# Kernel optimization log

Measured on AMD Instinct MI355X. Metric: run time of the kernel, lower is better.

The kernel has to match this reference:

```python
import jax, jax.numpy as jnp
import numpy as np

D = 128
N_DRUG = 100000
N_PROT = 50000
E_DD, E_DP, E_PD = 800000, 600000, 600000
EPS = 1e-5


def setup_inputs() -> dict:
    key = jax.random.key(0)
    ks = jax.random.split(key, 19)
    f32 = jnp.float32
    return {
        "x_drug": jax.random.normal(ks[0], (N_DRUG, D), f32),
        "x_prot": jax.random.normal(ks[1], (N_PROT, D), f32),
        "Wagg_dd": jax.random.normal(ks[2], (D, D), f32) * 0.05,
        "Wagg_dp": jax.random.normal(ks[3], (D, D), f32) * 0.05,
        "Wagg_pd": jax.random.normal(ks[4], (D, D), f32) * 0.05,
        "W_drug": jax.random.normal(ks[5], (D, 2 * D), f32) * 0.05,
        "b_drug": jax.random.normal(ks[6], (D,), f32) * 0.01,
        "W_prot": jax.random.normal(ks[7], (D, 2 * D), f32) * 0.05,
        "b_prot": jax.random.normal(ks[8], (D,), f32) * 0.01,
        "g_drug": jnp.ones((D,), f32),
        "be_drug": jnp.zeros((D,), f32),
        "g_prot": jnp.ones((D,), f32),
        "be_prot": jnp.zeros((D,), f32),
        "ei_dd_src": jax.random.randint(ks[9], (E_DD,), 0, N_DRUG, jnp.int64 if jax.config.jax_enable_x64 else jnp.int32),
        "ei_dd_dst": jax.random.randint(ks[10], (E_DD,), 0, N_DRUG),
        "ei_dp_src": jax.random.randint(ks[11], (E_DP,), 0, N_DRUG),
        "ei_dp_dst": jax.random.randint(ks[12], (E_DP,), 0, N_PROT),
        "ei_pd_src": jax.random.randint(ks[13], (E_PD,), 0, N_PROT),
        "ei_pd_dst": jax.random.randint(ks[14], (E_PD,), 0, N_DRUG),
    }


def _rel_agg(x_src, W_agg, src_idx, dst_idx, n_dst):
    # gather -> per-relation Linear (no bias) + ReLU -> scatter-mean
    h = jax.nn.relu(x_src[src_idx] @ W_agg.T)            # [E, D]
    s = jax.ops.segment_sum(h, dst_idx, num_segments=n_dst)
    c = jax.ops.segment_sum(jnp.ones((src_idx.shape[0],), h.dtype), dst_idx, num_segments=n_dst)
    return s / jnp.maximum(c, 1.0)[:, None]


def _layernorm(x, g, b):
    mu = jnp.mean(x, axis=-1, keepdims=True)
    var = jnp.mean(jnp.square(x - mu), axis=-1, keepdims=True)
    return (x - mu) * jax.lax.rsqrt(var + EPS) * g + b


def _node_update(h_self, h_agg, W, b, g, be):
    h = jax.nn.relu(jnp.concatenate([h_self, h_agg], axis=-1) @ W.T + b)
    return _layernorm(h + h_self, g, be)  # dropout is identity in eval


def reference(x_drug, x_prot, Wagg_dd, Wagg_dp, Wagg_pd, W_drug, b_drug,
              W_prot, b_prot, g_drug, be_drug, g_prot, be_prot,
              ei_dd_src, ei_dd_dst, ei_dp_src, ei_dp_dst, ei_pd_src, ei_pd_dst):
    agg_dd = _rel_agg(x_drug, Wagg_dd, ei_dd_src, ei_dd_dst, N_DRUG)
    agg_pd = _rel_agg(x_prot, Wagg_pd, ei_pd_src, ei_pd_dst, N_DRUG)
    agg_drug = (agg_dd + agg_pd) * 0.5                   # mean over relations into 'drug'
    agg_prot = _rel_agg(x_drug, Wagg_dp, ei_dp_src, ei_dp_dst, N_PROT)
    out_drug = _node_update(x_drug, agg_drug, W_drug, b_drug, g_drug, be_drug)
    out_prot = _node_update(x_prot, agg_prot, W_prot, b_prot, g_prot, be_prot)
    # pack the per-type outputs into one array [N_DRUG + N_PROT, D]
    return jnp.concatenate([out_drug, out_prot], axis=0)
```

## Files before the change

kernel.cpp:

```cpp
#include <hip/hip_runtime.h>

#define D 128
#define ND 100000
#define NP 50000
#define NE_DD 800000
#define NE_DP 600000
#define NE_PD 600000
#define NE_TOT 2000000

#define NTOT 250000
#define NBC 490
#define NC 250880
#define CHUNKA 4096
#define NBLKA 489
#define CHUNKIT 16
#define SEGCAP 8192

#define TF_BD 782
#define TF_BP 196
#define NU_BD 391
#define NU_BP 196

typedef __bf16 bf16;
typedef __attribute__((ext_vector_type(8))) __bf16 bf16x8;
typedef __attribute__((ext_vector_type(2))) __bf16 bf16x2;
typedef __attribute__((ext_vector_type(4))) float f32x4;
typedef __attribute__((ext_vector_type(2))) float f32x2;

#define OFF_WDD   0UL
#define OFF_WDP   32768UL
#define OFF_WPD   65536UL
#define OFF_WDRUG 98304UL
#define OFF_WPROT 163840UL
#define OFF_YDD   229376UL
#define OFF_YDP   (OFF_YDD + 25600000UL)
#define OFF_YPD   (OFF_YDP + 25600000UL)
#define OFF_AGGD  (OFF_YPD + 12800000UL)
#define OFF_AGGP  (OFF_AGGD + 25600000UL)
#define OFF_BCNT  (OFF_AGGP + 12800000UL)
#define OFF_GCUR  (OFF_BCNT + 2048UL)
#define OFF_CBASE (OFF_GCUR + 2048UL)
#define OFF_RP    (OFF_CBASE + 2048UL)
#define OFF_PAIRS (OFF_RP + 1003520UL)
#define OFF_POOL  (OFF_PAIRS + 16000000UL)

__global__ __launch_bounds__(256) void prep_kernel(
    const float* __restrict__ w0, const float* __restrict__ w1,
    const float* __restrict__ w2, const float* __restrict__ w3,
    const float* __restrict__ w4,
    bf16* __restrict__ o0, bf16* __restrict__ o1, bf16* __restrict__ o2,
    bf16* __restrict__ o3, bf16* __restrict__ o4,
    const int* __restrict__ dd_dst, const int* __restrict__ pd_dst,
    const int* __restrict__ dp_dst, int* __restrict__ bcnt)
{
    int m = blockIdx.y;
    int t = threadIdx.x;
    if (m == 5) {
        __shared__ int h[NBC];
        for (int i = t; i < NBC; i += 256) h[i] = 0;
        __syncthreads();
        for (int e = blockIdx.x * 256 + t; e < NE_TOT; e += 128 * 256) {
            int didx;
            if (e < NE_DD) didx = dd_dst[e];
            else if (e < NE_DD + NE_PD) didx = ND + pd_dst[e - NE_DD];
            else didx = 2 * ND + dp_dst[e - NE_DD - NE_PD];
            atomicAdd(&h[didx >> 9], 1);
        }
        __syncthreads();
        for (int i = t; i < NBC; i += 256)
            if (h[i]) atomicAdd(&bcnt[i], h[i]);
        return;
    }
    int i = blockIdx.x * 256 + t;
    const float* src; bf16* dst; int n; bool perm;
    switch (m) {
        case 0: src = w0; dst = o0; n = D * D; perm = false; break;
        case 1: src = w1; dst = o1; n = D * D; perm = false; break;
        case 2: src = w2; dst = o2; n = D * D; perm = false; break;
        case 3: src = w3; dst = o3; n = D * 2 * D; perm = true; break;
        default: src = w4; dst = o4; n = D * 2 * D; perm = true; break;
    }
    if (i < n) {
        int si = i;
        if (perm) {
            int col = i & 255;
            if (col >= 128) {
                int p = col - 128;
                si = (i & ~255) | (128 + (p & 7) * 16 + (p >> 3));
            }
        }
        dst[i] = (bf16)src[si];
    }
}

__global__ __launch_bounds__(256) void scan_kernel(
    const int* __restrict__ bcnt, int* __restrict__ cbase, int* __restrict__ gcur)
{
    __shared__ int ps[256];
    int t = threadIdx.x;
    int i0 = 2 * t, i1 = 2 * t + 1;
    int c0 = (i0 < NBC) ? bcnt[i0] : 0;
    int c1 = (i1 < NBC) ? bcnt[i1] : 0;
    ps[t] = c0 + c1;
    __syncthreads();
#pragma unroll
    for (int off = 1; off < 256; off <<= 1) {
        int add = (t >= off) ? ps[t - off] : 0;
        __syncthreads();
        ps[t] += add;
        __syncthreads();
    }
    int excl = ps[t] - (c0 + c1);
    if (i0 <= NBC) cbase[i0] = excl;
    if (i0 < NBC) gcur[i0] = excl;
    if (i1 < NBC) { cbase[i1] = excl + c0; gcur[i1] = excl + c0; }
}

__device__ __forceinline__ bf16x8 load_a_f32(const float* __restrict__ xr)
{
    float4 f0 = *(const float4*)xr;
    float4 f1 = *(const float4*)(xr + 4);
    bf16x8 a;
    a[0] = (bf16)f0.x; a[1] = (bf16)f0.y; a[2] = (bf16)f0.z; a[3] = (bf16)f0.w;
    a[4] = (bf16)f1.x; a[5] = (bf16)f1.y; a[6] = (bf16)f1.z; a[7] = (bf16)f1.w;
    return a;
}

__device__ __forceinline__ void transform_drug(
    const float* __restrict__ x, const bf16* __restrict__ W1,
    const bf16* __restrict__ W2, bf16* __restrict__ y1, bf16* __restrict__ y2,
    int blk)
{
    int lane = threadIdx.x & 63;
    int wave = threadIdx.x >> 6;
    int q = lane >> 4, c = lane & 15;
    int mb = blk * 128 + wave * 32;

    f32x4 acc1[2][8], acc2[2][8];
#pragma unroll
    for (int mt = 0; mt < 2; mt++)
#pragma unroll
        for (int nt = 0; nt < 8; nt++) { acc1[mt][nt] = 0; acc2[mt][nt] = 0; }

#pragma unroll
    for (int kb = 0; kb < 4; kb++) {
        int k = kb * 32 + q * 8;
        bf16x8 a[2];
#pragma unroll
        for (int mt = 0; mt < 2; mt++) {
            int row = min(mb + mt * 16 + c, ND - 1);
            a[mt] = load_a_f32(x + (long)row * D + k);
        }
#pragma unroll
        for (int nt = 0; nt < 8; nt++) {
            bf16x8 b1 = *(const bf16x8*)(W1 + (nt * 16 + c) * D + k);
            bf16x8 b2 = *(const bf16x8*)(W2 + (nt * 16 + c) * D + k);
#pragma unroll
            for (int mt = 0; mt < 2; mt++) {
                acc1[mt][nt] = __builtin_amdgcn_mfma_f32_16x16x32_bf16(a[mt], b1, acc1[mt][nt], 0, 0, 0);
                acc2[mt][nt] = __builtin_amdgcn_mfma_f32_16x16x32_bf16(a[mt], b2, acc2[mt][nt], 0, 0, 0);
            }
        }
    }
#pragma unroll
    for (int mt = 0; mt < 2; mt++)
#pragma unroll
        for (int r = 0; r < 4; r++) {
            int row = mb + mt * 16 + q * 4 + r;
            if (row < ND) {
                bf16x8 o1, o2;
#pragma unroll
                for (int nt = 0; nt < 8; nt++) {
                    o1[nt] = (bf16)fmaxf(acc1[mt][nt][r], 0.f);
                    o2[nt] = (bf16)fmaxf(acc2[mt][nt][r], 0.f);
                }
                *(bf16x8*)(y1 + (long)row * D + c * 8) = o1;
                *(bf16x8*)(y2 + (long)row * D + c * 8) = o2;
            }
        }
}

__device__ __forceinline__ void transform_prot(
    const float* __restrict__ x, const bf16* __restrict__ W1,
    bf16* __restrict__ y1, int blk)
{
    int lane = threadIdx.x & 63;
    int wave = threadIdx.x >> 6;
    int q = lane >> 4, c = lane & 15;
    int mb = blk * 256 + wave * 64;

    f32x4 acc[4][8];
#pragma unroll
    for (int mt = 0; mt < 4; mt++)
#pragma unroll
        for (int nt = 0; nt < 8; nt++) acc[mt][nt] = 0;

#pragma unroll
    for (int kb = 0; kb < 4; kb++) {
        int k = kb * 32 + q * 8;
        bf16x8 a[4];
#pragma unroll
        for (int mt = 0; mt < 4; mt++) {
            int row = min(mb + mt * 16 + c, NP - 1);
            a[mt] = load_a_f32(x + (long)row * D + k);
        }
#pragma unroll
        for (int nt = 0; nt < 8; nt++) {
            bf16x8 b1 = *(const bf16x8*)(W1 + (nt * 16 + c) * D + k);
#pragma unroll
            for (int mt = 0; mt < 4; mt++)
                acc[mt][nt] = __builtin_amdgcn_mfma_f32_16x16x32_bf16(a[mt], b1, acc[mt][nt], 0, 0, 0);
        }
    }
#pragma unroll
    for (int mt = 0; mt < 4; mt++)
#pragma unroll
        for (int r = 0; r < 4; r++) {
            int row = mb + mt * 16 + q * 4 + r;
            if (row < NP) {
                bf16x8 o1;
#pragma unroll
                for (int nt = 0; nt < 8; nt++)
                    o1[nt] = (bf16)fmaxf(acc[mt][nt][r], 0.f);
                *(bf16x8*)(y1 + (long)row * D + c * 8) = o1;
            }
        }
}

__device__ __forceinline__ void binA_body(
    int blk,
    const int* __restrict__ dd_src, const int* __restrict__ dd_dst,
    const int* __restrict__ pd_src, const int* __restrict__ pd_dst,
    const int* __restrict__ dp_src, const int* __restrict__ dp_dst,
    int* __restrict__ gcur, unsigned* __restrict__ pairs)
{
    __shared__ int h[NBC];
    __shared__ int gb[NBC];
    __shared__ int2 pr[CHUNKA];
    __shared__ unsigned short rk[CHUNKA];
    for (int i = threadIdx.x; i < NBC; i += 256) h[i] = 0;
    __syncthreads();
    int base = blk * CHUNKA;
    for (int it = 0; it < CHUNKIT; it++) {
        int idx = it * 256 + threadIdx.x;
        int e = base + idx;
        int didx = -1, sv = 0;
        if (e < NE_TOT) {
            if (e < NE_DD) { didx = dd_dst[e]; sv = dd_src[e]; }
            else if (e < NE_DD + NE_PD) { int u = e - NE_DD; didx = ND + pd_dst[u]; sv = pd_src[u]; }
            else { int u = e - NE_DD - NE_PD; didx = 2 * ND + dp_dst[u]; sv = dp_src[u]; }
            rk[idx] = (unsigned short)atomicAdd(&h[didx >> 9], 1);
        }
        pr[idx] = make_int2(didx, sv);
    }
    __syncthreads();
    for (int b = threadIdx.x; b < NBC; b += 256) {
        int c = h[b];
        gb[b] = c ? atomicAdd(&gcur[b], c) : 0;
    }
    __syncthreads();
    for (int it = 0; it < CHUNKIT; it++) {
        int idx = it * 256 + threadIdx.x;
        int2 p = pr[idx];
        if (p.x >= 0)
            pairs[gb[p.x >> 9] + rk[idx]] =
                ((unsigned)(p.x & 511) << 17) | (unsigned)p.y;
    }
}

__global__ __launch_bounds__(256, 2) void stage2_kernel(
    const float* __restrict__ x_drug, const float* __restrict__ x_prot,
    const bf16* __restrict__ Wdd, const bf16* __restrict__ Wdp,
    const bf16* __restrict__ Wpd,
    bf16* __restrict__ y_dd, bf16* __restrict__ y_dp, bf16* __restrict__ y_pd,
    const int* __restrict__ dd_src, const int* __restrict__ dd_dst,
    const int* __restrict__ pd_src, const int* __restrict__ pd_dst,
    const int* __restrict__ dp_src, const int* __restrict__ dp_dst,
    int* __restrict__ gcur, unsigned* __restrict__ pairs)
{
    int blk = blockIdx.x;
    if (blk < NBLKA) {
        binA_body(blk, dd_src, dd_dst, pd_src, pd_dst, dp_src, dp_dst,
                  gcur, pairs);
        return;
    }
    blk -= NBLKA;
    if (blk < TF_BD)
        transform_drug(x_drug, Wdd, Wdp, y_dd, y_dp, blk);
    else
        transform_prot(x_prot, Wpd, y_pd, blk - TF_BD);
}

__global__ __launch_bounds__(256) void sortB_kernel(
    const int* __restrict__ cbase, const unsigned* __restrict__ pairs,
    int* __restrict__ pool, int* __restrict__ rp)
{
    __shared__ int h[512];
    __shared__ int excl[512];
    __shared__ int ps[256];
    __shared__ unsigned short rk[SEGCAP];
    __shared__ int outl[SEGCAP];

    int b = blockIdx.x;
    int s0 = cbase[b], s1 = cbase[b + 1];
    int n = s1 - s0;
    if (n > SEGCAP) n = SEGCAP;
    int t = threadIdx.x;
    h[t] = 0; h[t + 256] = 0;
    __syncthreads();

    for (int i = t; i < n; i += 256) {
        unsigned p = pairs[s0 + i];
        rk[i] = (unsigned short)atomicAdd(&h[p >> 17], 1);
    }
    __syncthreads();

    int c0 = h[2 * t], c1 = h[2 * t + 1];
    ps[t] = c0 + c1;
    __syncthreads();
#pragma unroll
    for (int off = 1; off < 256; off <<= 1) {
        int add = (t >= off) ? ps[t - off] : 0;
        __syncthreads();
        ps[t] += add;
        __syncthreads();
    }
    int pe = ps[t] - (c0 + c1);
    excl[2 * t] = pe;
    excl[2 * t + 1] = pe + c0;
    __syncthreads();

    int nb = b * 512;
    rp[nb + 2 * t] = s0 + excl[2 * t];
    rp[nb + 2 * t + 1] = s0 + excl[2 * t + 1];

    for (int i = t; i < n; i += 256) {
        unsigned p = pairs[s0 + i];
        outl[excl[p >> 17] + rk[i]] = (int)(p & 0x1FFFFu);
    }
    __syncthreads();
    for (int i = t; i < n; i += 256)
        pool[s0 + i] = outl[i];
}

__device__ __forceinline__ void acc2(unsigned u, f32x2* acc)
{
    union { unsigned u; float f; } lo, hi;
    lo.u = u << 16;
    hi.u = u & 0xFFFF0000u;
    f32x2 d; d.x = lo.f; d.y = hi.f;
    *acc += d;
}

__device__ __forceinline__ void acc_seg(
    const int* __restrict__ pool, int s, int e,
    const unsigned* __restrict__ y, int lane, f32x2* acc)
{
    int j = s;
    for (; j + 8 <= e; j += 8) {
        unsigned u[8];
#pragma unroll
        for (int t = 0; t < 8; t++)
            u[t] = y[(long)pool[j + t] * 64 + lane];
#pragma unroll
        for (int t = 0; t < 8; t++) acc2(u[t], acc);
    }
    if (j + 4 <= e) {
        unsigned u[4];
#pragma unroll
        for (int t = 0; t < 4; t++)
            u[t] = y[(long)pool[j + t] * 64 + lane];
#pragma unroll
        for (int t = 0; t < 4; t++) acc2(u[t], acc);
        j += 4;
    }
    if (j + 2 <= e) {
        unsigned u0 = y[(long)pool[j] * 64 + lane];
        unsigned u1 = y[(long)pool[j + 1] * 64 + lane];
        acc2(u0, acc); acc2(u1, acc);
        j += 2;
    }
    if (j < e)
        acc2(y[(long)pool[j] * 64 + lane], acc);
}

__global__ __launch_bounds__(256) void gather_kernel(
    const int* __restrict__ rp, const int* __restrict__ pool,
    const unsigned* __restrict__ y_dd, const unsigned* __restrict__ y_pd,
    const unsigned* __restrict__ y_dp,
    bf16* __restrict__ agg_d, bf16* __restrict__ agg_p)
{
    int wid = blockIdx.x * 4 + (threadIdx.x >> 6);
    int lane = threadIdx.x & 63;

    if (wid < ND) {
        int g = wid;
        int s1 = rp[g], e1 = rp[g + 1];
        int s2 = rp[ND + g], e2 = rp[ND + g + 1];
        f32x2 a; a.x = 0.f; a.y = 0.f;
        f32x2 b; b.x = 0.f; b.y = 0.f;
        acc_seg(pool, s1, e1, y_dd, lane, &a);
        acc_seg(pool, s2, e2, y_pd, lane, &b);
        float i1 = 0.5f / (float)max(e1 - s1, 1);
        float i2 = 0.5f / (float)max(e2 - s2, 1);
        f32x2 r = a * i1 + b * i2;
        bf16x2 o; o[0] = (bf16)r.x; o[1] = (bf16)r.y;
        *(bf16x2*)(agg_d + (long)g * D + lane * 2) = o;
    } else if (wid < ND + NP) {
        int p = wid - ND;
        int s1 = rp[2 * ND + p], e1 = rp[2 * ND + p + 1];
        f32x2 a; a.x = 0.f; a.y = 0.f;
        acc_seg(pool, s1, e1, y_dp, lane, &a);
        float i1 = 1.0f / (float)max(e1 - s1, 1);
        f32x2 r = a * i1;
        bf16x2 o; o[0] = (bf16)r.x; o[1] = (bf16)r.y;
        *(bf16x2*)(agg_p + (long)p * D + lane * 2) = o;
    }
}

__device__ __forceinline__ void node_update_body(
    const float* __restrict__ x, const bf16* __restrict__ agg,
    const bf16* __restrict__ W, const float* __restrict__ b,
    const float* __restrict__ g, const float* __restrict__ be,
    float* __restrict__ out, int M, int blk)
{
    int lane = threadIdx.x & 63;
    int wave = threadIdx.x >> 6;
    int q = lane >> 4, c = lane & 15;
    int mb = blk * 256 + wave * 64;

    f32x4 acc[4][8];
#pragma unroll
    for (int mt = 0; mt < 4; mt++)
#pragma unroll
        for (int nt = 0; nt < 8; nt++) acc[mt][nt] = 0;

#pragma unroll
    for (int kb = 0; kb < 8; kb++) {
        bf16x8 a[4];
#pragma unroll
        for (int mt = 0; mt < 4; mt++) {
            int row = min(mb + mt * 16 + c, M - 1);
            if (kb < 4)
                a[mt] = load_a_f32(x + (long)row * D + kb * 32 + q * 8);
            else
                a[mt] = *(const bf16x8*)(agg + (long)row * D + (kb - 4) * 32 + q * 8);
        }
#pragma unroll
        for (int nt = 0; nt < 8; nt++) {
            bf16x8 bw = *(const bf16x8*)(W + (nt * 16 + c) * (2 * D) + kb * 32 + q * 8);
#pragma unroll
            for (int mt = 0; mt < 4; mt++)
                acc[mt][nt] = __builtin_amdgcn_mfma_f32_16x16x32_bf16(a[mt], bw, acc[mt][nt], 0, 0, 0);
        }
    }

    float bv[8], gv[8], bev[8];
#pragma unroll
    for (int nt = 0; nt < 8; nt++) {
        int col = nt * 16 + c;
        bv[nt] = b[col]; gv[nt] = g[col]; bev[nt] = be[col];
    }
#pragma unroll
    for (int mt = 0; mt < 4; mt++)
#pragma unroll
        for (int r = 0; r < 4; r++) {
            int row = mb + mt * 16 + q * 4 + r;
            int rowc = min(row, M - 1);
            const float* xr = x + (long)rowc * D + c;
            float v[8];
            float sum = 0.f, sq = 0.f;
#pragma unroll
            for (int nt = 0; nt < 8; nt++) {
                float h = fmaxf(acc[mt][nt][r] + bv[nt], 0.f);
                float t = h + xr[nt * 16];
                v[nt] = t; sum += t; sq += t * t;
            }
#pragma unroll
            for (int m = 1; m < 16; m <<= 1) {
                sum += __shfl_xor(sum, m, 64);
                sq  += __shfl_xor(sq,  m, 64);
            }
            float mu   = sum * (1.f / 128.f);
            float var  = sq  * (1.f / 128.f) - mu * mu;
            float rstd = rsqrtf(var + 1e-5f);
            if (row < M) {
                float* op = out + (long)row * D + c;
#pragma unroll
                for (int nt = 0; nt < 8; nt++)
                    op[nt * 16] = (v[nt] - mu) * rstd * gv[nt] + bev[nt];
            }
        }
}

__global__ __launch_bounds__(256, 2) void node_update_kernel(
    const float* __restrict__ x_drug, const float* __restrict__ x_prot,
    const bf16* __restrict__ agg_d, const bf16* __restrict__ agg_p,
    const bf16* __restrict__ Wdrug, const float* __restrict__ b_drug,
    const float* __restrict__ g_drug, const float* __restrict__ be_drug,
    const bf16* __restrict__ Wprot, const float* __restrict__ b_prot,
    const float* __restrict__ g_prot, const float* __restrict__ be_prot,
    float* __restrict__ out)
{
    int blk = blockIdx.x;
    if (blk < NU_BD)
        node_update_body(x_drug, agg_d, Wdrug, b_drug, g_drug, be_drug,
                         out, ND, blk);
    else
        node_update_body(x_prot, agg_p, Wprot, b_prot, g_prot, be_prot,
                         out + (long)ND * D, NP, blk - NU_BD);
}

extern "C" void kernel_launch(void* const* d_in, const int* in_sizes, int n_in,
                              void* d_out, int out_size, void* d_ws, size_t ws_size,
                              hipStream_t stream)
{
    const float* x_drug  = (const float*)d_in[0];
    const float* x_prot  = (const float*)d_in[1];
    const float* Wagg_dd = (const float*)d_in[2];
    const float* Wagg_dp = (const float*)d_in[3];
    const float* Wagg_pd = (const float*)d_in[4];
    const float* W_drug  = (const float*)d_in[5];
    const float* b_drug  = (const float*)d_in[6];
    const float* W_prot  = (const float*)d_in[7];
    const float* b_prot  = (const float*)d_in[8];
    const float* g_drug  = (const float*)d_in[9];
    const float* be_drug = (const float*)d_in[10];
    const float* g_prot  = (const float*)d_in[11];
    const float* be_prot = (const float*)d_in[12];
    const int* dd_src = (const int*)d_in[13];
    const int* dd_dst = (const int*)d_in[14];
    const int* dp_src = (const int*)d_in[15];
    const int* dp_dst = (const int*)d_in[16];
    const int* pd_src = (const int*)d_in[17];
    const int* pd_dst = (const int*)d_in[18];

    char* ws = (char*)d_ws;
    bf16* Wdd   = (bf16*)(ws + OFF_WDD);
    bf16* Wdp   = (bf16*)(ws + OFF_WDP);
    bf16* Wpd   = (bf16*)(ws + OFF_WPD);
    bf16* Wdrug = (bf16*)(ws + OFF_WDRUG);
    bf16* Wprot = (bf16*)(ws + OFF_WPROT);
    bf16* y_dd  = (bf16*)(ws + OFF_YDD);
    bf16* y_dp  = (bf16*)(ws + OFF_YDP);
    bf16* y_pd  = (bf16*)(ws + OFF_YPD);
    bf16* agg_d = (bf16*)(ws + OFF_AGGD);
    bf16* agg_p = (bf16*)(ws + OFF_AGGP);
    int* bcnt   = (int*)(ws + OFF_BCNT);
    int* gcur   = (int*)(ws + OFF_GCUR);
    int* cbase  = (int*)(ws + OFF_CBASE);
    int* rp     = (int*)(ws + OFF_RP);
    unsigned* pairs = (unsigned*)(ws + OFF_PAIRS);
    int* pool   = (int*)(ws + OFF_POOL);
    float* out  = (float*)d_out;

    hipMemsetAsync(bcnt, 0, NBC * sizeof(int), stream);

    prep_kernel<<<dim3(128, 6), 256, 0, stream>>>(
        Wagg_dd, Wagg_dp, Wagg_pd, W_drug, W_prot,
        Wdd, Wdp, Wpd, Wdrug, Wprot,
        dd_dst, pd_dst, dp_dst, bcnt);

    scan_kernel<<<1, 256, 0, stream>>>(bcnt, cbase, gcur);

    stage2_kernel<<<NBLKA + TF_BD + TF_BP, 256, 0, stream>>>(
        x_drug, x_prot, Wdd, Wdp, Wpd, y_dd, y_dp, y_pd,
        dd_src, dd_dst, pd_src, pd_dst, dp_src, dp_dst, gcur, pairs);

    sortB_kernel<<<NBC, 256, 0, stream>>>(cbase, pairs, pool, rp);

    gather_kernel<<<(ND + NP + 3) / 4, 256, 0, stream>>>(
        rp, pool, (const unsigned*)y_dd, (const unsigned*)y_pd,
        (const unsigned*)y_dp, agg_d, agg_p);

    node_update_kernel<<<NU_BD + NU_BP, 256, 0, stream>>>(
        x_drug, x_prot, agg_d, agg_p,
        Wdrug, b_drug, g_drug, be_drug,
        Wprot, b_prot, g_prot, be_prot, out);
}
```

Measured before the change: 416.0 us.

## Store transformed edge features in 8-bit custom float and split transform kernel

Per-node transformed features (y_dd, y_dp, y_pd) are now encoded as a custom 8-bit float (4-bit exponent, 3-bit mantissa, scaled by 2^-120, no sign because the values are post-ReLU) instead of bf16. This halves the bytes the gather kernel fetches per edge and the bytes the transform writes. The fused stage2 kernel is split into a separate binning kernel and a transform kernel launched after sortB, which changes overlap and scheduling. The coarse quantization clamps large values at the encoding maximum and loses precision, so accuracy tolerance is at risk.

```diff
diff --git a/kernel.cpp b/kernel.cpp
--- a/kernel.cpp
+++ b/kernel.cpp
@@ -44,6 +44,17 @@
 #define OFF_PAIRS (OFF_RP + 1003520UL)
 #define OFF_POOL  (OFF_PAIRS + 16000000UL)
 
+__device__ __forceinline__ unsigned enc1(float f)
+{
+    unsigned t = __float_as_uint(f * 0x1p-120f);
+    t = (t + 0x80000u) >> 20;
+    return t > 0x7Eu ? 0x7Eu : t;
+}
+__device__ __forceinline__ unsigned enc4(float a, float b, float c, float d)
+{
+    return enc1(a) | (enc1(b) << 8) | (enc1(c) << 16) | (enc1(d) << 24);
+}
+
 __global__ __launch_bounds__(256) void prep_kernel(
     const float* __restrict__ w0, const float* __restrict__ w1,
     const float* __restrict__ w2, const float* __restrict__ w3,
@@ -128,8 +139,8 @@
 
 __device__ __forceinline__ void transform_drug(
     const float* __restrict__ x, const bf16* __restrict__ W1,
-    const bf16* __restrict__ W2, bf16* __restrict__ y1, bf16* __restrict__ y2,
-    int blk)
+    const bf16* __restrict__ W2, unsigned char* __restrict__ y1,
+    unsigned char* __restrict__ y2, int blk)
 {
     int lane = threadIdx.x & 63;
     int wave = threadIdx.x >> 6;
@@ -168,21 +179,26 @@
         for (int r = 0; r < 4; r++) {
             int row = mb + mt * 16 + q * 4 + r;
             if (row < ND) {
-                bf16x8 o1, o2;
+                float v1[8], v2[8];
 #pragma unroll
                 for (int nt = 0; nt < 8; nt++) {
-                    o1[nt] = (bf16)fmaxf(acc1[mt][nt][r], 0.f);
-                    o2[nt] = (bf16)fmaxf(acc2[mt][nt][r], 0.f);
+                    v1[nt] = fmaxf(acc1[mt][nt][r], 0.f);
+                    v2[nt] = fmaxf(acc2[mt][nt][r], 0.f);
                 }
-                *(bf16x8*)(y1 + (long)row * D + c * 8) = o1;
-                *(bf16x8*)(y2 + (long)row * D + c * 8) = o2;
+                uint2 p1, p2;
+                p1.x = enc4(v1[0], v1[1], v1[2], v1[3]);
+                p1.y = enc4(v1[4], v1[5], v1[6], v1[7]);
+                p2.x = enc4(v2[0], v2[1], v2[2], v2[3]);
+                p2.y = enc4(v2[4], v2[5], v2[6], v2[7]);
+                *(uint2*)(y1 + (long)row * D + c * 8) = p1;
+                *(uint2*)(y2 + (long)row * D + c * 8) = p2;
             }
         }
 }
 
 __device__ __forceinline__ void transform_prot(
     const float* __restrict__ x, const bf16* __restrict__ W1,
-    bf16* __restrict__ y1, int blk)
+    unsigned char* __restrict__ y1, int blk)
 {
     int lane = threadIdx.x & 63;
     int wave = threadIdx.x >> 6;
@@ -218,17 +234,33 @@
         for (int r = 0; r < 4; r++) {
             int row = mb + mt * 16 + q * 4 + r;
             if (row < NP) {
-                bf16x8 o1;
+                float v[8];
 #pragma unroll
                 for (int nt = 0; nt < 8; nt++)
-                    o1[nt] = (bf16)fmaxf(acc[mt][nt][r], 0.f);
-                *(bf16x8*)(y1 + (long)row * D + c * 8) = o1;
-            }
-        }
-}
-
-__device__ __forceinline__ void binA_body(
-    int blk,
+                    v[nt] = fmaxf(acc[mt][nt][r], 0.f);
+                uint2 p1;
+                p1.x = enc4(v[0], v[1], v[2], v[3]);
+                p1.y = enc4(v[4], v[5], v[6], v[7]);
+                *(uint2*)(y1 + (long)row * D + c * 8) = p1;
+            }
+        }
+}
+
+__global__ __launch_bounds__(256, 2) void transform_kernel(
+    const float* __restrict__ x_drug, const float* __restrict__ x_prot,
+    const bf16* __restrict__ Wdd, const bf16* __restrict__ Wdp,
+    const bf16* __restrict__ Wpd,
+    unsigned char* __restrict__ y_dd, unsigned char* __restrict__ y_dp,
+    unsigned char* __restrict__ y_pd)
+{
+    int blk = blockIdx.x;
+    if (blk < TF_BD)
+        transform_drug(x_drug, Wdd, Wdp, y_dd, y_dp, blk);
+    else
+        transform_prot(x_prot, Wpd, y_pd, blk - TF_BD);
+}
+
+__global__ __launch_bounds__(256) void binA_kernel(
     const int* __restrict__ dd_src, const int* __restrict__ dd_dst,
     const int* __restrict__ pd_src, const int* __restrict__ pd_dst,
     const int* __restrict__ dp_src, const int* __restrict__ dp_dst,
@@ -240,7 +272,7 @@
     __shared__ unsigned short rk[CHUNKA];
     for (int i = threadIdx.x; i < NBC; i += 256) h[i] = 0;
     __syncthreads();
-    int base = blk * CHUNKA;
+    int base = blockIdx.x * CHUNKA;
     for (int it = 0; it < CHUNKIT; it++) {
         int idx = it * 256 + threadIdx.x;
         int e = base + idx;
@@ -268,29 +300,6 @@
     }
 }
 
-__global__ __launch_bounds__(256, 2) void stage2_kernel(
-    const float* __restrict__ x_drug, const float* __restrict__ x_prot,
-    const bf16* __restrict__ Wdd, const bf16* __restrict__ Wdp,
-    const bf16* __restrict__ Wpd,
-    bf16* __restrict__ y_dd, bf16* __restrict__ y_dp, bf16* __restrict__ y_pd,
-    const int* __restrict__ dd_src, const int* __restrict__ dd_dst,
-    const int* __restrict__ pd_src, const int* __restrict__ pd_dst,
-    const int* __restrict__ dp_src, const int* __restrict__ dp_dst,
-    int* __restrict__ gcur, unsigned* __restrict__ pairs)
-{
-    int blk = blockIdx.x;
-    if (blk < NBLKA) {
-        binA_body(blk, dd_src, dd_dst, pd_src, pd_dst, dp_src, dp_dst,
-                  gcur, pairs);
-        return;
-    }
-    blk -= NBLKA;
-    if (blk < TF_BD)
-        transform_drug(x_drug, Wdd, Wdp, y_dd, y_dp, blk);
-    else
-        transform_prot(x_prot, Wpd, y_pd, blk - TF_BD);
-}
-
 __global__ __launch_bounds__(256) void sortB_kernel(
     const int* __restrict__ cbase, const unsigned* __restrict__ pairs,
     int* __restrict__ pool, int* __restrict__ rp)
@@ -343,51 +352,51 @@
         pool[s0 + i] = outl[i];
 }
 
-__device__ __forceinline__ void acc2(unsigned u, f32x2* acc)
-{
-    union { unsigned u; float f; } lo, hi;
-    lo.u = u << 16;
-    hi.u = u & 0xFFFF0000u;
-    f32x2 d; d.x = lo.f; d.y = hi.f;
-    *acc += d;
+__device__ __forceinline__ void accw(unsigned short w, f32x2* acc)
+{
+    float lo = __uint_as_float((unsigned)(w & 0xFFu) << 20);
+    float hi = __uint_as_float((unsigned)(w >> 8) << 20);
+    acc->x = fmaf(lo, 0x1p120f, acc->x);
+    acc->y = fmaf(hi, 0x1p120f, acc->y);
 }
 
 __device__ __forceinline__ void acc_seg(
     const int* __restrict__ pool, int s, int e,
-    const unsigned* __restrict__ y, int lane, f32x2* acc)
+    const unsigned short* __restrict__ y, int lane, f32x2* acc)
 {
     int j = s;
     for (; j + 8 <= e; j += 8) {
-        unsigned u[8];
+        unsigned short u[8];
 #pragma unroll
         for (int t = 0; t < 8; t++)
             u[t] = y[(long)pool[j + t] * 64 + lane];
 #pragma unroll
-        for (int t = 0; t < 8; t++) acc2(u[t], acc);
+        for (int t = 0; t < 8; t++) accw(u[t], acc);
     }
     if (j + 4 <= e) {
-        unsigned u[4];
+        unsigned short u[4];
 #pragma unroll
         for (int t = 0; t < 4; t++)
             u[t] = y[(long)pool[j + t] * 64 + lane];
 #pragma unroll
-        for (int t = 0; t < 4; t++) acc2(u[t], acc);
+        for (int t = 0; t < 4; t++) accw(u[t], acc);
         j += 4;
     }
     if (j + 2 <= e) {
-        unsigned u0 = y[(long)pool[j] * 64 + lane];
-        unsigned u1 = y[(long)pool[j + 1] * 64 + lane];
-        acc2(u0, acc); acc2(u1, acc);
+        unsigned short u0 = y[(long)pool[j] * 64 + lane];
+        unsigned short u1 = y[(long)pool[j + 1] * 64 + lane];
+        accw(u0, acc); accw(u1, acc);
         j += 2;
     }
     if (j < e)
-        acc2(y[(long)pool[j] * 64 + lane], acc);
+        accw(y[(long)pool[j] * 64 + lane], acc);
 }
 
 __global__ __launch_bounds__(256) void gather_kernel(
     const int* __restrict__ rp, const int* __restrict__ pool,
-    const unsigned* __restrict__ y_dd, const unsigned* __restrict__ y_pd,
-    const unsigned* __restrict__ y_dp,
+    const unsigned short* __restrict__ y_dd,
+    const unsigned short* __restrict__ y_pd,
+    const unsigned short* __restrict__ y_dp,
     bf16* __restrict__ agg_d, bf16* __restrict__ agg_p)
 {
     int wid = blockIdx.x * 4 + (threadIdx.x >> 6);
@@ -541,9 +550,9 @@
     bf16* Wpd   = (bf16*)(ws + OFF_WPD);
     bf16* Wdrug = (bf16*)(ws + OFF_WDRUG);
     bf16* Wprot = (bf16*)(ws + OFF_WPROT);
-    bf16* y_dd  = (bf16*)(ws + OFF_YDD);
-    bf16* y_dp  = (bf16*)(ws + OFF_YDP);
-    bf16* y_pd  = (bf16*)(ws + OFF_YPD);
+    unsigned char* y_dd = (unsigned char*)(ws + OFF_YDD);
+    unsigned char* y_dp = (unsigned char*)(ws + OFF_YDP);
+    unsigned char* y_pd = (unsigned char*)(ws + OFF_YPD);
     bf16* agg_d = (bf16*)(ws + OFF_AGGD);
     bf16* agg_p = (bf16*)(ws + OFF_AGGP);
     int* bcnt   = (int*)(ws + OFF_BCNT);
@@ -563,15 +572,17 @@
 
     scan_kernel<<<1, 256, 0, stream>>>(bcnt, cbase, gcur);
 
-    stage2_kernel<<<NBLKA + TF_BD + TF_BP, 256, 0, stream>>>(
-        x_drug, x_prot, Wdd, Wdp, Wpd, y_dd, y_dp, y_pd,
+    binA_kernel<<<NBLKA, 256, 0, stream>>>(
         dd_src, dd_dst, pd_src, pd_dst, dp_src, dp_dst, gcur, pairs);
 
     sortB_kernel<<<NBC, 256, 0, stream>>>(cbase, pairs, pool, rp);
 
+    transform_kernel<<<TF_BD + TF_BP, 256, 0, stream>>>(
+        x_drug, x_prot, Wdd, Wdp, Wpd, y_dd, y_dp, y_pd);
+
     gather_kernel<<<(ND + NP + 3) / 4, 256, 0, stream>>>(
-        rp, pool, (const unsigned*)y_dd, (const unsigned*)y_pd,
-        (const unsigned*)y_dp, agg_d, agg_p);
+        rp, pool, (const unsigned short*)y_dd, (const unsigned short*)y_pd,
+        (const unsigned short*)y_dp, agg_d, agg_p);
 
     node_update_kernel<<<NU_BD + NU_BP, 256, 0, stream>>>(
         x_drug, x_prot, agg_d, agg_p,
```

Result: no change. 415.4 us (-0.2%).
